# Kernel tuning notes

Measured on AMD Instinct MI355X. Metric: run time of the kernel, lower is better.

## Reference

```python
import jax, jax.numpy as jnp
import numpy as np

B, T, I, H, N, M, O = 256, 128, 512, 512, 1024, 512, 512
EPS = 1e-8


def setup_inputs() -> dict:
    key = jax.random.key(0)
    ks = jax.random.split(key, 10)
    rn = lambda k, shape, s: jax.random.normal(k, shape, jnp.float32) * s
    s_h, s_i, s_m = 1.0 / np.sqrt(H), 1.0 / np.sqrt(I), 1.0 / np.sqrt(M)
    return {
        "x": jax.random.normal(ks[0], (B, T, 1, I), jnp.float32),
        "mem0": jnp.full((N, M), 1e-6, jnp.float32),          # memory init fill_(1e-6)
        "wr0": jnp.eye(B, N, dtype=jnp.float32),               # torch.eye(batch, N)
        "ww0": jnp.eye(B, N, dtype=jnp.float32),
        "h0": rn(ks[1], (B, H), 1.0 / H),                      # normal_(0, 1/num_hidden)
        "Wx": rn(ks[2], (I, H), s_i),
        "Wr": rn(ks[3], (M, H), s_m),
        "bh": jnp.zeros((H,), jnp.float32),
        "Whr": rn(ks[4], (H, M + 6), s_h),                      # read head: k,beta,g,s(3),gamma
        "bhr": jnp.zeros((M + 6,), jnp.float32),
        "Whw": rn(ks[5], (H, M + 6), s_h),                      # write head addressing
        "bhw": jnp.zeros((M + 6,), jnp.float32),
        "Wea": rn(ks[6], (H, 2 * M), s_h),                      # write head erase/add
        "bea": jnp.zeros((2 * M,), jnp.float32),
        "Wo": rn(ks[7], (H, O), s_h),
        "bo": jnp.zeros((O,), jnp.float32),
    }


def _address(h, w_prev, mem, Wh, bh_):
    # Standard NTM addressing: content -> interpolate -> shift -> sharpen.
    p = h @ Wh + bh_                                   # (B, M+6)
    k = jnp.tanh(p[:, :M])                             # key (B, M)
    beta = jax.nn.softplus(p[:, M:M + 1])              # strength >= 0
    g = jax.nn.sigmoid(p[:, M + 1:M + 2])              # gate in (0,1)
    s = jax.nn.softmax(p[:, M + 2:M + 5], axis=-1)     # shift over {-1,0,+1}
    gamma = 1.0 + jax.nn.softplus(p[:, M + 5:M + 6])   # sharpen >= 1
    kn = k / (jnp.linalg.norm(k, axis=-1, keepdims=True) + EPS)
    mn = mem / (jnp.linalg.norm(mem, axis=-1, keepdims=True) + EPS)
    wc = jax.nn.softmax(beta * (kn @ mn.T), axis=-1)   # content weights (B, N)
    wg = g * wc + (1.0 - g) * w_prev                   # interpolation (strictly > 0)
    wt = (s[:, 0:1] * jnp.roll(wg, -1, axis=1)
          + s[:, 1:2] * wg
          + s[:, 2:3] * jnp.roll(wg, 1, axis=1))       # circular shift conv
    wp = wt ** gamma
    return wp / (jnp.sum(wp, axis=-1, keepdims=True) + EPS)


def reference(x, mem0, wr0, ww0, h0, Wx, Wr, bh, Whr, bhr, Whw, bhw, Wea, bea, Wo, bo):
    xs = jnp.transpose(x[:, :, 0, :], (1, 0, 2))       # (T, B, I): x.permute(1,0,2,3)

    def step(carry, x_t):
        mem, wr, ww, h = carry
        # write head (get_weights=False): erase/add into memory with prev ww
        ea = h @ Wea + bea
        e = jax.nn.sigmoid(ea[:, :M])                  # (B, M)
        a = jnp.tanh(ea[:, M:])                        # (B, M)
        mem = (mem * (1.0 - jnp.einsum('bn,bm->nm', ww, e) / B)
               + jnp.einsum('bn,bm->nm', ww, a) / B)   # batch-averaged, mem shared (N, M)
        # read head (get_weights=False): r = wr @ M
        r = wr @ mem                                   # (B, M)
        # controller.step(x_t, r)
        h = jnp.tanh(x_t @ Wx + r @ Wr + bh)           # (B, H)
        # new addressing weights from updated hidden + updated memory
        ww = _address(h, ww, mem, Whw, bhw)
        wr = _address(h, wr, mem, Whr, bhr)
        out = jax.nn.sigmoid(h @ Wo + bo)              # (B, O)
        return (mem, wr, ww, h), out

    _, outs = jax.lax.scan(step, (mem0, wr0, ww0, h0), xs)  # outs (T, B, O)
    return jnp.transpose(outs, (1, 0, 2))              # (B, T, O)
```

## Files before the change

kernel.cpp:

```cpp
#include <hip/hip_runtime.h>
#include <math.h>

#define B_ 256
#define T_ 128
#define I_ 512
#define H_ 512
#define N_ 1024
#define M_ 512
#define O_ 512
#define EPS_ 1e-8f

typedef unsigned short u16;
typedef __attribute__((ext_vector_type(8))) short v8s;
typedef __attribute__((ext_vector_type(4))) float v4f;

#define MFMA(a, b, c) __builtin_amdgcn_mfma_f32_16x16x32_bf16(a, b, c, 0, 0, 0)

#define PL_BIG 1310720
#define PL_WXT 262144
#define PL_WRT 262144
#define PL_MEM 524288
#define PL_W   262144
#define PL_H   131072
#define PL_KH  262144

__device__ __forceinline__ float sigm_(float x) { return 1.f / (1.f + expf(-x)); }
__device__ __forceinline__ float softplus_(float x) { return x > 20.f ? x : log1pf(expf(x)); }
__device__ __forceinline__ u16 f2bf(float f) {
    unsigned u = __float_as_uint(f);
    u += 0x7fffu + ((u >> 16) & 1u);
    return (u16)(u >> 16);
}
__device__ __forceinline__ float bf2f(u16 h) { return __uint_as_float((unsigned)h << 16); }
__device__ __forceinline__ void split2(float f, u16& h, u16& m) {
    h = f2bf(f);
    m = f2bf(f - bf2f(h));
}

__device__ __forceinline__ float wave_sum_(float v) {
#pragma unroll
    for (int o = 32; o > 0; o >>= 1) v += __shfl_down(v, o);
    return v;
}
__device__ __forceinline__ float wave_max_(float v) {
#pragma unroll
    for (int o = 32; o > 0; o >>= 1) v = fmaxf(v, __shfl_down(v, o));
    return v;
}
__device__ float block_sum_(float v, float* s) {
    int lane = threadIdx.x & 63, wid = threadIdx.x >> 6, nw = blockDim.x >> 6;
    v = wave_sum_(v);
    if (lane == 0) s[wid] = v;
    __syncthreads();
    float r = (threadIdx.x < nw) ? s[threadIdx.x] : 0.f;
    if (wid == 0) { r = wave_sum_(r); if (lane == 0) s[0] = r; }
    __syncthreads();
    float out = s[0];
    __syncthreads();
    return out;
}
__device__ float block_max_(float v, float* s) {
    int lane = threadIdx.x & 63, wid = threadIdx.x >> 6, nw = blockDim.x >> 6;
    v = wave_max_(v);
    if (lane == 0) s[wid] = v;
    __syncthreads();
    float r = (threadIdx.x < nw) ? s[threadIdx.x] : -3.4e38f;
    if (wid == 0) { r = wave_max_(r); if (lane == 0) s[0] = r; }
    __syncthreads();
    float out = s[0];
    __syncthreads();
    return out;
}

struct EpiEA0 {
    const float* bea; u16* eT; u16* aT;
    __device__ void operator()(int r0, int c, v4f v) const {
#pragma unroll
        for (int r = 0; r < 4; r++) {
            float val = v[r] + bea[c];
            u16* dst;
            int b = r0 + r;
            if (c < M_) { val = sigm_(val); dst = eT + (size_t)c * B_ + b; }
            else        { val = tanhf(val); dst = aT + (size_t)(c - M_) * B_ + b; }
            u16 h, m; split2(val, h, m);
            dst[0] = h; dst[PL_H] = m;
        }
    }
};
struct EpiR {
    u16* rp;
    __device__ void operator()(int r0, int c, v4f v) const {
#pragma unroll
        for (int r = 0; r < 4; r++) {
            u16 h, m; split2(v[r], h, m);
            size_t idx = (size_t)(r0 + r) * M_ + c;
            rp[idx] = h; rp[PL_H + idx] = m;
        }
    }
};
struct EpiH {
    const float* xwxt; const float* bh; float* hf; u16* hp;
    __device__ void operator()(int r0, int c, v4f v) const {
#pragma unroll
        for (int r = 0; r < 4; r++) {
            int b = r0 + r;
            float val = tanhf(v[r] + xwxt[(size_t)b * (T_ * O_) + c] + bh[c]);
            size_t idx = (size_t)b * H_ + c;
            hf[idx] = val;
            u16 h, m; split2(val, h, m);
            hp[idx] = h; hp[PL_H + idx] = m;
        }
    }
};
struct EpiFused {
    const float* bhw; const float* bhr; const float* bo; const float* bea;
    u16* khp; float* outt; u16* eT; u16* aT;
    __device__ void operator()(int r0, int c, v4f v) const {
        if (c < 1024) {
            int head = c >> 9, key = c & 511;
            const float* bb = head ? bhr : bhw;
#pragma unroll
            for (int r = 0; r < 4; r++) {
                float val = tanhf(v[r] + bb[key]);
                size_t idx = (size_t)(head * 256 + r0 + r) * M_ + key;
                u16 h, m; split2(val, h, m);
                khp[idx] = h; khp[PL_KH + idx] = m;
            }
        } else if (c < 1536) {
            int o = c - 1024;
#pragma unroll
            for (int r = 0; r < 4; r++)
                outt[(size_t)(r0 + r) * (T_ * O_) + o] = sigm_(v[r] + bo[o]);
        } else {
            int m = c - 1536;
#pragma unroll
            for (int r = 0; r < 4; r++) {
                float val = v[r] + bea[m];
                u16* dst;
                int b = r0 + r;
                if (m < M_) { val = sigm_(val); dst = eT + (size_t)m * B_ + b; }
                else        { val = tanhf(val); dst = aT + (size_t)(m - M_) * B_ + b; }
                u16 h, mm; split2(val, h, mm);
                dst[0] = h; dst[PL_H] = mm;
            }
        }
    }
};

template <int TM, class Epi>
__global__ __launch_bounds__(256) void gemm2(const u16* __restrict__ Ap, int lda, int apl,
                                             const u16* __restrict__ Bp, int ldb, int bpl,
                                             int K, Epi epi) {
    constexpr int AL = (TM * 32 * 2) / (256 * 8);
    constexpr int MT = TM / 32;
    __shared__ u16 As[2][TM][40];
    __shared__ u16 Bs[2][64][40];
    const int tid = threadIdx.x, lane = tid & 63, w = tid >> 6;
    const int wy = w >> 1, wx = w & 1, q = lane >> 4, l15 = lane & 15;
    const int row0 = blockIdx.y * TM, col0 = blockIdx.x * 64;
    uint4 ra[AL], rb[2];
    auto loadA = [&](int k0) {
#pragma unroll
        for (int j = 0; j < AL; j++) {
            int s = j * 256 + tid, p = s / (TM * 4), rr = (s >> 2) % TM, kg = s & 3;
            ra[j] = *(const uint4*)(Ap + (size_t)p * apl + (size_t)(row0 + rr) * lda + k0 + kg * 8);
        }
    };
    auto loadB = [&](int k0) {
#pragma unroll
        for (int j = 0; j < 2; j++) {
            int s = j * 256 + tid, p = s >> 8, rr = (s >> 2) & 63, kg = s & 3;
            rb[j] = *(const uint4*)(Bp + (size_t)p * bpl + (size_t)(col0 + rr) * ldb + k0 + kg * 8);
        }
    };
    v4f acc[MT][2] = {};
    loadA(0); loadB(0);
    for (int k0 = 0; k0 < K; k0 += 32) {
#pragma unroll
        for (int j = 0; j < AL; j++) {
            int s = j * 256 + tid, p = s / (TM * 4), rr = (s >> 2) % TM, kg = s & 3;
            *(uint4*)&As[p][rr][kg * 8] = ra[j];
        }
#pragma unroll
        for (int j = 0; j < 2; j++) {
            int s = j * 256 + tid, p = s >> 8, rr = (s >> 2) & 63, kg = s & 3;
            *(uint4*)&Bs[p][rr][kg * 8] = rb[j];
        }
        __syncthreads();
        if (k0 + 32 < K) { loadA(k0 + 32); loadB(k0 + 32); }
        v8s af[MT][2], bf[2][2];
#pragma unroll
        for (int mt = 0; mt < MT; mt++) {
            af[mt][0] = *(const v8s*)&As[0][wy * (TM / 2) + mt * 16 + l15][q * 8];
            af[mt][1] = *(const v8s*)&As[1][wy * (TM / 2) + mt * 16 + l15][q * 8];
        }
#pragma unroll
        for (int nt = 0; nt < 2; nt++) {
            bf[nt][0] = *(const v8s*)&Bs[0][wx * 32 + nt * 16 + l15][q * 8];
            bf[nt][1] = *(const v8s*)&Bs[1][wx * 32 + nt * 16 + l15][q * 8];
        }
#pragma unroll
        for (int mt = 0; mt < MT; mt++)
#pragma unroll
            for (int nt = 0; nt < 2; nt++) {
                v4f c = acc[mt][nt];
                c = MFMA(af[mt][0], bf[nt][0], c);
                c = MFMA(af[mt][0], bf[nt][1], c);
                c = MFMA(af[mt][1], bf[nt][0], c);
                acc[mt][nt] = c;
            }
        __syncthreads();
    }
#pragma unroll
    for (int mt = 0; mt < MT; mt++)
#pragma unroll
        for (int nt = 0; nt < 2; nt++)
            epi(row0 + wy * (TM / 2) + mt * 16 + q * 4, col0 + wx * 32 + nt * 16 + l15, acc[mt][nt]);
}

__global__ __launch_bounds__(256) void memupd2(const u16* __restrict__ wwT, const u16* __restrict__ eT,
                                               const u16* __restrict__ aT, float* __restrict__ memf,
                                               u16* __restrict__ mem_pl, u16* __restrict__ memT_pl,
                                               float* __restrict__ ssqp) {
    __shared__ u16 As[2][64][40], Be[2][64][40], Ba[2][64][40];
    __shared__ float ssqs[64];
    const int tid = threadIdx.x, lane = tid & 63, w = tid >> 6;
    const int wy = w >> 1, wx = w & 1, q = lane >> 4, l15 = lane & 15;
    const int row0 = blockIdx.y * 64, col0 = blockIdx.x * 64;
    if (tid < 64) ssqs[tid] = 0.f;
    uint4 rA[2], rE[2], rB[2];
    auto loadAll = [&](int k0) {
#pragma unroll
        for (int j = 0; j < 2; j++) {
            int s = j * 256 + tid, p = s >> 8, rr = (s >> 2) & 63, kg = s & 3;
            rA[j] = *(const uint4*)(wwT + (size_t)p * PL_W + (size_t)(row0 + rr) * B_ + k0 + kg * 8);
            rE[j] = *(const uint4*)(eT + (size_t)p * PL_H + (size_t)(col0 + rr) * B_ + k0 + kg * 8);
            rB[j] = *(const uint4*)(aT + (size_t)p * PL_H + (size_t)(col0 + rr) * B_ + k0 + kg * 8);
        }
    };
    v4f ae[2][2] = {}, aa[2][2] = {};
    loadAll(0);
    for (int k0 = 0; k0 < B_; k0 += 32) {
#pragma unroll
        for (int j = 0; j < 2; j++) {
            int s = j * 256 + tid, p = s >> 8, rr = (s >> 2) & 63, kg = s & 3;
            *(uint4*)&As[p][rr][kg * 8] = rA[j];
            *(uint4*)&Be[p][rr][kg * 8] = rE[j];
            *(uint4*)&Ba[p][rr][kg * 8] = rB[j];
        }
        __syncthreads();
        if (k0 + 32 < B_) loadAll(k0 + 32);
        v8s af[2][2], be[2][2], ba[2][2];
#pragma unroll
        for (int mt = 0; mt < 2; mt++) {
            af[mt][0] = *(const v8s*)&As[0][wy * 32 + mt * 16 + l15][q * 8];
            af[mt][1] = *(const v8s*)&As[1][wy * 32 + mt * 16 + l15][q * 8];
            be[mt][0] = *(const v8s*)&Be[0][wx * 32 + mt * 16 + l15][q * 8];
            be[mt][1] = *(const v8s*)&Be[1][wx * 32 + mt * 16 + l15][q * 8];
            ba[mt][0] = *(const v8s*)&Ba[0][wx * 32 + mt * 16 + l15][q * 8];
            ba[mt][1] = *(const v8s*)&Ba[1][wx * 32 + mt * 16 + l15][q * 8];
        }
#pragma unroll
        for (int mt = 0; mt < 2; mt++)
#pragma unroll
            for (int nt = 0; nt < 2; nt++) {
                v4f c = ae[mt][nt];
                c = MFMA(af[mt][0], be[nt][0], c);
                c = MFMA(af[mt][0], be[nt][1], c);
                c = MFMA(af[mt][1], be[nt][0], c);
                ae[mt][nt] = c;
                v4f d = aa[mt][nt];
                d = MFMA(af[mt][0], ba[nt][0], d);
                d = MFMA(af[mt][0], ba[nt][1], d);
                d = MFMA(af[mt][1], ba[nt][0], d);
                aa[mt][nt] = d;
            }
        __syncthreads();
    }
    const float invB = 1.f / (float)B_;
#pragma unroll
    for (int mt = 0; mt < 2; mt++)
#pragma unroll
        for (int nt = 0; nt < 2; nt++) {
            int r0 = row0 + wy * 32 + mt * 16 + q * 4;
            int c  = col0 + wx * 32 + nt * 16 + l15;
            u16 hv[4][2];
#pragma unroll
            for (int r = 0; r < 4; r++) {
                size_t idx = (size_t)(r0 + r) * M_ + c;
                float old = memf[idx];
                float nv = old * (1.f - ae[mt][nt][r] * invB) + aa[mt][nt][r] * invB;
                memf[idx] = nv;
                u16 h, m; split2(nv, h, m);
                mem_pl[idx] = h; mem_pl[PL_MEM + idx] = m;
                hv[r][0] = h; hv[r][1] = m;
                atomicAdd(&ssqs[r0 + r - row0], nv * nv);
            }
            size_t tb = (size_t)c * N_ + r0;
            *(ushort4*)&memT_pl[tb] = make_ushort4(hv[0][0], hv[1][0], hv[2][0], hv[3][0]);
            *(ushort4*)&memT_pl[PL_MEM + tb] = make_ushort4(hv[0][1], hv[1][1], hv[2][1], hv[3][1]);
        }
    __syncthreads();
    if (tid < 64) ssqp[(size_t)(row0 + tid) * 8 + blockIdx.x] = ssqs[tid];
}

__global__ __launch_bounds__(256) void logits2(const u16* __restrict__ khp, const u16* __restrict__ memp,
                                               const float* __restrict__ ssqp, float* __restrict__ logits) {
    __shared__ u16 As[2][64][40], Bs[2][64][40];
    __shared__ float invn_s[64];
    const int tid = threadIdx.x, lane = tid & 63, w = tid >> 6;
    const int wy = w >> 1, wx = w & 1, q = lane >> 4, l15 = lane & 15;
    const int row0 = blockIdx.y * 64, col0 = blockIdx.x * 64;
    if (tid < 64) {
        float s = 0.f;
#pragma unroll
        for (int j = 0; j < 8; j++) s += ssqp[(size_t)(col0 + tid) * 8 + j];
        invn_s[tid] = 1.f / (sqrtf(s) + EPS_);
    }
    uint4 ra[2], rb[2];
    auto loadAll = [&](int k0) {
#pragma unroll
        for (int j = 0; j < 2; j++) {
            int s = j * 256 + tid, p = s >> 8, rr = (s >> 2) & 63, kg = s & 3;
            ra[j] = *(const uint4*)(khp + (size_t)p * PL_KH + (size_t)(row0 + rr) * M_ + k0 + kg * 8);
            rb[j] = *(const uint4*)(memp + (size_t)p * PL_MEM + (size_t)(col0 + rr) * M_ + k0 + kg * 8);
        }
    };
    v4f acc[2][2] = {};
    loadAll(0);
    for (int k0 = 0; k0 < M_; k0 += 32) {
#pragma unroll
        for (int j = 0; j < 2; j++) {
            int s = j * 256 + tid, p = s >> 8, rr = (s >> 2) & 63, kg = s & 3;
            *(uint4*)&As[p][rr][kg * 8] = ra[j];
            *(uint4*)&Bs[p][rr][kg * 8] = rb[j];
        }
        __syncthreads();
        if (k0 + 32 < M_) loadAll(k0 + 32);
        v8s af[2][2], bf[2][2];
#pragma unroll
        for (int mt = 0; mt < 2; mt++) {
            af[mt][0] = *(const v8s*)&As[0][wy * 32 + mt * 16 + l15][q * 8];
            af[mt][1] = *(const v8s*)&As[1][wy * 32 + mt * 16 + l15][q * 8];
            bf[mt][0] = *(const v8s*)&Bs[0][wx * 32 + mt * 16 + l15][q * 8];
            bf[mt][1] = *(const v8s*)&Bs[1][wx * 32 + mt * 16 + l15][q * 8];
        }
#pragma unroll
        for (int mt = 0; mt < 2; mt++)
#pragma unroll
            for (int nt = 0; nt < 2; nt++) {
                v4f c = acc[mt][nt];
                c = MFMA(af[mt][0], bf[nt][0], c);
                c = MFMA(af[mt][0], bf[nt][1], c);
                c = MFMA(af[mt][1], bf[nt][0], c);
                acc[mt][nt] = c;
            }
        __syncthreads();
    }
#pragma unroll
    for (int mt = 0; mt < 2; mt++)
#pragma unroll
        for (int nt = 0; nt < 2; nt++) {
            int r0 = row0 + wy * 32 + mt * 16 + q * 4;
            int c  = col0 + wx * 32 + nt * 16 + l15;
            float in_ = invn_s[c - col0];
#pragma unroll
            for (int r = 0; r < 4; r++)
                logits[(size_t)(r0 + r) * N_ + c] = acc[mt][nt][r] * in_;
        }
}

__global__ __launch_bounds__(256) void gemm2_xwx(const float* __restrict__ x, const u16* __restrict__ WxT,
                                                 float* __restrict__ outbuf) {
    __shared__ u16 As[2][64][40];
    __shared__ u16 Bs[2][64][40];
    const int tid = threadIdx.x, lane = tid & 63, w = tid >> 6;
    const int wy = w >> 1, wx = w & 1, q = lane >> 4, l15 = lane & 15;
    const int row0 = blockIdx.y * 64, col0 = blockIdx.x * 64;
    const int sr = tid >> 2, ss = (tid & 3) * 8;
    const int arow = row0 + sr, ab = arow & 255, at = arow >> 8;
    const float* Asrc = x + ((size_t)ab * T_ + at) * I_ + ss;
    v4f acc[2][2] = {};
    for (int k0 = 0; k0 < I_; k0 += 32) {
        float4 f0 = *(const float4*)(Asrc + k0);
        float4 f1 = *(const float4*)(Asrc + k0 + 4);
        float av8[8] = {f0.x, f0.y, f0.z, f0.w, f1.x, f1.y, f1.z, f1.w};
#pragma unroll
        for (int j = 0; j < 8; j++) {
            u16 h, m; split2(av8[j], h, m);
            As[0][sr][ss + j] = h; As[1][sr][ss + j] = m;
        }
#pragma unroll
        for (int p = 0; p < 2; p++)
            *(uint4*)&Bs[p][sr][ss] = *(const uint4*)&WxT[(size_t)p * PL_WXT + (size_t)(col0 + sr) * I_ + k0 + ss];
        __syncthreads();
        v8s af[2][2], bf[2][2];
#pragma unroll
        for (int mt = 0; mt < 2; mt++) {
            af[mt][0] = *(const v8s*)&As[0][wy * 32 + mt * 16 + l15][q * 8];
            af[mt][1] = *(const v8s*)&As[1][wy * 32 + mt * 16 + l15][q * 8];
            bf[mt][0] = *(const v8s*)&Bs[0][wx * 32 + mt * 16 + l15][q * 8];
            bf[mt][1] = *(const v8s*)&Bs[1][wx * 32 + mt * 16 + l15][q * 8];
        }
#pragma unroll
        for (int mt = 0; mt < 2; mt++)
#pragma unroll
            for (int nt = 0; nt < 2; nt++) {
                v4f c = acc[mt][nt];
                c = MFMA(af[mt][0], bf[nt][0], c);
                c = MFMA(af[mt][0], bf[nt][1], c);
                c = MFMA(af[mt][1], bf[nt][0], c);
                acc[mt][nt] = c;
            }
        __syncthreads();
    }
#pragma unroll
    for (int mt = 0; mt < 2; mt++)
#pragma unroll
        for (int nt = 0; nt < 2; nt++) {
            int r0 = row0 + wy * 32 + mt * 16 + q * 4;
            int c  = col0 + wx * 32 + nt * 16 + l15;
#pragma unroll
            for (int r = 0; r < 4; r++) {
                int row = r0 + r, b = row & 255, t = row >> 8;
                outbuf[((size_t)b * T_ + t) * O_ + c] = acc[mt][nt][r];
            }
        }
}

__global__ __launch_bounds__(256) void decomp_t(const float* __restrict__ in, int ldin, int c0,
                                                int R, u16* __restrict__ outp, int opl) {
    __shared__ float Ls[32][33];
    const int r0 = blockIdx.x * 32, cB = blockIdx.y * 32;
    const int tid = threadIdx.x;
    int lr = tid >> 3, lc = (tid & 7) * 4;
#pragma unroll
    for (int j = 0; j < 4; j++)
        Ls[lr][lc + j] = in[(size_t)(r0 + lr) * ldin + c0 + cB + lc + j];
    __syncthreads();
    int lc2 = tid >> 3, lr2 = (tid & 7) * 4;
    u16 hv[4], mv[4];
#pragma unroll
    for (int j = 0; j < 4; j++) split2(Ls[lr2 + j][lc2], hv[j], mv[j]);
    size_t base = (size_t)(cB + lc2) * R + r0 + lr2;
    *(ushort4*)&outp[0 * (size_t)opl + base] = make_ushort4(hv[0], hv[1], hv[2], hv[3]);
    *(ushort4*)&outp[1 * (size_t)opl + base] = make_ushort4(mv[0], mv[1], mv[2], mv[3]);
}

__global__ __launch_bounds__(512) void wh6_kernel(const float* __restrict__ Whw, const float* __restrict__ Whr,
                                                  float* __restrict__ w6w, float* __restrict__ w6r) {
    int k = threadIdx.x;
    const float* src = blockIdx.x ? Whr : Whw;
    float* dst = blockIdx.x ? w6r : w6w;
#pragma unroll
    for (int j = 0; j < 6; j++) dst[k * 6 + j] = src[(size_t)k * (M_ + 6) + M_ + j];
}
__global__ __launch_bounds__(256) void init_mem(const float* __restrict__ mem0, float* __restrict__ memf,
                                                u16* __restrict__ mem_pl, u16* __restrict__ memT_pl) {
    int n = blockIdx.x;
    for (int c = threadIdx.x; c < M_; c += 256) {
        float v = mem0[(size_t)n * M_ + c];
        size_t idx = (size_t)n * M_ + c;
        memf[idx] = v;
        u16 h, m; split2(v, h, m);
        mem_pl[idx] = h; mem_pl[PL_MEM + idx] = m;
        size_t tb = (size_t)c * N_ + n;
        memT_pl[tb] = h; memT_pl[PL_MEM + tb] = m;
    }
}
__global__ __launch_bounds__(256) void init_w(const float* __restrict__ wr0, const float* __restrict__ ww0,
                                              float* __restrict__ wrf, float* __restrict__ wwf,
                                              u16* __restrict__ wr_pl, u16* __restrict__ wwT_pl) {
    int b = blockIdx.x;
    for (int n = threadIdx.x; n < N_; n += 256) {
        size_t idx = (size_t)b * N_ + n;
        float vw = ww0[idx]; wwf[idx] = vw;
        u16 h, m; split2(vw, h, m);
        size_t tb = (size_t)n * B_ + b;
        wwT_pl[tb] = h; wwT_pl[PL_W + tb] = m;
        float vr = wr0[idx]; wrf[idx] = vr;
        split2(vr, h, m);
        wr_pl[idx] = h; wr_pl[PL_W + idx] = m;
    }
}
__global__ __launch_bounds__(64) void init_h(const float* __restrict__ h0, float* __restrict__ hf,
                                             u16* __restrict__ hp) {
    int b = blockIdx.x;
    for (int c = threadIdx.x; c < H_; c += 64) {
        size_t idx = (size_t)b * H_ + c;
        float v = h0[idx];
        hf[idx] = v;
        u16 h, m; split2(v, h, m);
        hp[idx] = h; hp[PL_H + idx] = m;
    }
}

__global__ __launch_bounds__(256) void addr_k2(const float* __restrict__ logits, const float* __restrict__ hf,
                                               const float* __restrict__ w6w, const float* __restrict__ w6r,
                                               const float* __restrict__ bhw, const float* __restrict__ bhr,
                                               const u16* __restrict__ khp,
                                               float* __restrict__ wwf, float* __restrict__ wrf,
                                               u16* __restrict__ wwT_pl, u16* __restrict__ wr_pl) {
    __shared__ float wgs[N_];
    __shared__ float red[8];
    int row = blockIdx.x, head = row >> 8, b = row & 255;
    const float* w6 = head ? w6r : w6w;
    const float* bias = head ? bhr : bhw;
    float* wf = head ? wrf : wwf;
    int tid = threadIdx.x;
    float d0 = 0, d1 = 0, d2 = 0, d3 = 0, d4 = 0, d5 = 0, ssq = 0;
#pragma unroll
    for (int j = 0; j < 2; j++) {
        int k = tid + j * 256;
        float hv = hf[(size_t)b * H_ + k];
        const float* wk = w6 + k * 6;
        d0 += hv * wk[0]; d1 += hv * wk[1]; d2 += hv * wk[2];
        d3 += hv * wk[3]; d4 += hv * wk[4]; d5 += hv * wk[5];
        size_t ki = (size_t)row * M_ + k;
        float kv = bf2f(khp[ki]) + bf2f(khp[PL_KH + ki]);
        ssq += kv * kv;
    }
    d0 = block_sum_(d0, red); d1 = block_sum_(d1, red); d2 = block_sum_(d2, red);
    d3 = block_sum_(d3, red); d4 = block_sum_(d4, red); d5 = block_sum_(d5, red);
    ssq = block_sum_(ssq, red);
    float beta = softplus_(d0 + bias[M_]);
    float g = sigm_(d1 + bias[M_ + 1]);
    float a0 = d2 + bias[M_ + 2], a1 = d3 + bias[M_ + 3], a2 = d4 + bias[M_ + 4];
    float mx3 = fmaxf(a0, fmaxf(a1, a2));
    float e0 = expf(a0 - mx3), e1 = expf(a1 - mx3), e2 = expf(a2 - mx3);
    float es = e0 + e1 + e2;
    float s0 = e0 / es, s1 = e1 / es, s2 = e2 / es;
    float gamma = 1.f + softplus_(d5 + bias[M_ + 5]);
    float rowsc = beta / (sqrtf(ssq) + EPS_);
    float l[4];
#pragma unroll
    for (int j = 0; j < 4; j++) l[j] = logits[(size_t)row * N_ + tid * 4 + j] * rowsc;
    float mx = fmaxf(fmaxf(l[0], l[1]), fmaxf(l[2], l[3]));
    mx = block_max_(mx, red);
    float ex[4], sum = 0.f;
#pragma unroll
    for (int j = 0; j < 4; j++) { ex[j] = expf(l[j] - mx); sum += ex[j]; }
    sum = block_sum_(sum, red);
    float inv = 1.f / sum;
    float wprev[4];
#pragma unroll
    for (int j = 0; j < 4; j++) wprev[j] = wf[(size_t)b * N_ + tid * 4 + j];
#pragma unroll
    for (int j = 0; j < 4; j++) wgs[tid * 4 + j] = g * ex[j] * inv + (1.f - g) * wprev[j];
    __syncthreads();
    float wp[4], psum = 0.f;
#pragma unroll
    for (int j = 0; j < 4; j++) {
        int n = tid * 4 + j;
        float wt = s0 * wgs[(n + 1) & (N_ - 1)] + s1 * wgs[n] + s2 * wgs[(n - 1) & (N_ - 1)];
        float v = expf(gamma * logf(wt));
        wp[j] = v; psum += v;
    }
    psum = block_sum_(psum, red);
    float invp = 1.f / (psum + EPS_);
#pragma unroll
    for (int j = 0; j < 4; j++) {
        int n = tid * 4 + j;
        float val = wp[j] * invp;
        wf[(size_t)b * N_ + n] = val;
        u16 h, m; split2(val, h, m);
        if (head == 0) {
            size_t tb = (size_t)n * B_ + b;
            wwT_pl[tb] = h; wwT_pl[PL_W + tb] = m;
        } else {
            size_t idx = (size_t)b * N_ + n;
            wr_pl[idx] = h; wr_pl[PL_W + idx] = m;
        }
    }
}

extern "C" void kernel_launch(void* const* d_in, const int* in_sizes, int n_in,
                              void* d_out, int out_size, void* d_ws, size_t ws_size,
                              hipStream_t stream) {
    (void)in_sizes; (void)n_in; (void)out_size; (void)ws_size;
    const float* x    = (const float*)d_in[0];
    const float* mem0 = (const float*)d_in[1];
    const float* wr0  = (const float*)d_in[2];
    const float* ww0  = (const float*)d_in[3];
    const float* h0   = (const float*)d_in[4];
    const float* Wx   = (const float*)d_in[5];
    const float* Wr   = (const float*)d_in[6];
    const float* bh   = (const float*)d_in[7];
    const float* Whr  = (const float*)d_in[8];
    const float* bhr  = (const float*)d_in[9];
    const float* Whw  = (const float*)d_in[10];
    const float* bhw  = (const float*)d_in[11];
    const float* Wea  = (const float*)d_in[12];
    const float* bea  = (const float*)d_in[13];
    const float* Wo   = (const float*)d_in[14];
    const float* bo   = (const float*)d_in[15];
    float* out = (float*)d_out;

    char* wsb = (char*)d_ws;
    size_t off = 0;
    auto carveU = [&](size_t elems) { u16* p = (u16*)(wsb + off); off += elems * sizeof(u16); return p; };
    u16* BigT    = carveU(2 * (size_t)PL_BIG);
    u16* WxT     = carveU(2 * (size_t)PL_WXT);
    u16* WrT     = carveU(2 * (size_t)PL_WRT);
    u16* mem_pl  = carveU(2 * (size_t)PL_MEM);
    u16* memT_pl = carveU(2 * (size_t)PL_MEM);
    u16* wwT_pl  = carveU(2 * (size_t)PL_W);
    u16* wr_pl   = carveU(2 * (size_t)PL_W);
    u16* h_pl    = carveU(2 * (size_t)PL_H);
    u16* r_pl    = carveU(2 * (size_t)PL_H);
    u16* eT_pl   = carveU(2 * (size_t)PL_H);
    u16* aT_pl   = carveU(2 * (size_t)PL_H);
    u16* kh_pl   = carveU(2 * (size_t)PL_KH);
    auto carveF = [&](size_t elems) { float* p = (float*)(wsb + off); off += elems * sizeof(float); return p; };
    float* memf   = carveF((size_t)N_ * M_);
    float* wwf    = carveF((size_t)B_ * N_);
    float* wrf    = carveF((size_t)B_ * N_);
    float* hf     = carveF((size_t)B_ * H_);
    float* logits = carveF((size_t)2 * B_ * N_);
    float* ssqp   = carveF((size_t)N_ * 8);
    float* w6w    = carveF(H_ * 6);
    float* w6r    = carveF(H_ * 6);

    decomp_t<<<dim3(16, 16), 256, 0, stream>>>(Whw, M_ + 6, 0, 512, BigT, PL_BIG);
    decomp_t<<<dim3(16, 16), 256, 0, stream>>>(Whr, M_ + 6, 0, 512, BigT + (size_t)512 * 512, PL_BIG);
    decomp_t<<<dim3(16, 16), 256, 0, stream>>>(Wo, 512, 0, 512, BigT + (size_t)1024 * 512, PL_BIG);
    decomp_t<<<dim3(16, 32), 256, 0, stream>>>(Wea, 1024, 0, 512, BigT + (size_t)1536 * 512, PL_BIG);
    decomp_t<<<dim3(16, 16), 256, 0, stream>>>(Wx, 512, 0, 512, WxT, PL_WXT);
    decomp_t<<<dim3(16, 16), 256, 0, stream>>>(Wr, 512, 0, 512, WrT, PL_WRT);
    wh6_kernel<<<2, 512, 0, stream>>>(Whw, Whr, w6w, w6r);
    init_mem<<<N_, 256, 0, stream>>>(mem0, memf, mem_pl, memT_pl);
    init_w<<<B_, 256, 0, stream>>>(wr0, ww0, wrf, wwf, wr_pl, wwT_pl);
    init_h<<<B_, 64, 0, stream>>>(h0, hf, h_pl);
    gemm2_xwx<<<dim3(8, 512), 256, 0, stream>>>(x, WxT, out);
    gemm2<32, EpiEA0><<<dim3(16, 8), 256, 0, stream>>>(
        h_pl, 512, PL_H, BigT + (size_t)1536 * 512, 512, PL_BIG, 512, EpiEA0{bea, eT_pl, aT_pl});

    for (int t = 0; t < T_; t++) {
        memupd2<<<dim3(8, 16), 256, 0, stream>>>(wwT_pl, eT_pl, aT_pl, memf, mem_pl, memT_pl, ssqp);
        gemm2<32, EpiR><<<dim3(8, 8), 256, 0, stream>>>(
            wr_pl, 1024, PL_W, memT_pl, 1024, PL_MEM, 1024, EpiR{r_pl});
        gemm2<32, EpiH><<<dim3(8, 8), 256, 0, stream>>>(
            r_pl, 512, PL_H, WrT, 512, PL_WRT, 512, EpiH{out + (size_t)t * O_, bh, hf, h_pl});
        gemm2<32, EpiFused><<<dim3(40, 8), 256, 0, stream>>>(
            h_pl, 512, PL_H, BigT, 512, PL_BIG, 512,
            EpiFused{bhw, bhr, bo, bea, kh_pl, out + (size_t)t * O_, eT_pl, aT_pl});
        logits2<<<dim3(16, 8), 256, 0, stream>>>(kh_pl, mem_pl, ssqp, logits);
        addr_k2<<<2 * B_, 256, 0, stream>>>(logits, hf, w6w, w6r, bhw, bhr, kh_pl,
                                            wwf, wrf, wwT_pl, wr_pl);
    }
}
```

Baseline: 17.68 ms.

## Fuse per-step kernels into a cooperative persistent megakernel with grid syncs

Replaces the six kernel launches per timestep with one cooperative persistent kernel that runs six phases separated by grid-wide syncs, with a per-phase launch fallback. The r and h GEMMs become split-K tiles accumulated with atomics into fp32 buffers. The tanh for h is recomputed inside the consumer phases instead of being stored, and wr is split into bf16 planes on the fly. The aim is to remove launch overhead and raise parallelism for small per-step GEMMs. In exchange it adds grid-sync cost, atomic traffic, and occupancy limits from the combined shared-memory footprint.

```diff
diff --git a/kernel.cpp b/kernel.cpp
--- a/kernel.cpp
+++ b/kernel.cpp
@@ -1,5 +1,8 @@
 #include <hip/hip_runtime.h>
+#include <hip/hip_cooperative_groups.h>
 #include <math.h>
+
+namespace cg = cooperative_groups;
 
 #define B_ 256
 #define T_ 128
@@ -36,6 +39,11 @@
     h = f2bf(f);
     m = f2bf(f - bf2f(h));
 }
+__device__ __forceinline__ void mfma3(v4f& c, v8s a0, v8s a1, v8s b0, v8s b1) {
+    c = MFMA(a0, b0, c);
+    c = MFMA(a0, b1, c);
+    c = MFMA(a1, b0, c);
+}
 
 __device__ __forceinline__ float wave_sum_(float v) {
 #pragma unroll
@@ -70,6 +78,422 @@
     float out = s[0];
     __syncthreads();
     return out;
+}
+
+struct Sh {
+    u16 sA[2 * 32 * 40];
+    u16 sB[2 * 64 * 40];
+    u16 sB2[2 * 64 * 40];
+    float wgs[N_];
+    float red[8];
+    float ssq[32];
+};
+
+struct MArgs {
+    const float *bea, *bh, *bhw, *bhr, *bo, *w6w, *w6r;
+    const u16 *BigT, *WrT;
+    u16 *mem_pl, *memT_pl, *wwT_pl, *eT, *aT, *kh;
+    float *memf, *wwf, *wrf, *r_acc, *h_acc, *xwx_cur, *logits, *ssqp, *outbuf;
+};
+
+__device__ void phase1(const MArgs& A, Sh& sh, int u, int t) {
+    const int tid = threadIdx.x;
+    if (u >= 256) {
+        int j = u - 256;
+        if (tid < 128) {
+            float4 z = make_float4(0.f, 0.f, 0.f, 0.f);
+            *(float4*)&A.r_acc[(size_t)j * 512 + tid * 4] = z;
+            *(float4*)&A.h_acc[(size_t)j * 512 + tid * 4] = z;
+            *(float4*)&A.xwx_cur[(size_t)j * 512 + tid * 4] =
+                *(const float4*)&A.outbuf[((size_t)j * T_ + t) * O_ + tid * 4];
+        }
+        return;
+    }
+    const int lane = tid & 63, w = tid >> 6, wy = w >> 1, wx = w & 1, q = lane >> 4, l15 = lane & 15;
+    const int n0 = (u >> 3) * 32, m0c = (u & 7) * 64;
+    if (tid < 32) sh.ssq[tid] = 0.f;
+    const int ap = tid >> 7, ar = (tid >> 2) & 31, akg = tid & 3;
+    uint4 pa, pb[2], pc[2];
+    auto ld = [&](int k0) {
+        pa = *(const uint4*)(A.wwT_pl + (size_t)ap * PL_W + (size_t)(n0 + ar) * B_ + k0 + akg * 8);
+#pragma unroll
+        for (int j = 0; j < 2; j++) {
+            int s = j * 256 + tid, p = s >> 8, rr = (s >> 2) & 63, kg = s & 3;
+            pb[j] = *(const uint4*)(A.eT + (size_t)p * PL_H + (size_t)(m0c + rr) * B_ + k0 + kg * 8);
+            pc[j] = *(const uint4*)(A.aT + (size_t)p * PL_H + (size_t)(m0c + rr) * B_ + k0 + kg * 8);
+        }
+    };
+    v4f ae[2] = {}, aa[2] = {};
+    ld(0);
+    for (int k0 = 0; k0 < B_; k0 += 32) {
+        *(uint4*)&sh.sA[(ap * 32 + ar) * 40 + akg * 8] = pa;
+#pragma unroll
+        for (int j = 0; j < 2; j++) {
+            int s = j * 256 + tid, p = s >> 8, rr = (s >> 2) & 63, kg = s & 3;
+            *(uint4*)&sh.sB[(p * 64 + rr) * 40 + kg * 8] = pb[j];
+            *(uint4*)&sh.sB2[(p * 64 + rr) * 40 + kg * 8] = pc[j];
+        }
+        __syncthreads();
+        if (k0 + 32 < B_) ld(k0 + 32);
+        v8s a0 = *(const v8s*)&sh.sA[(0 * 32 + wy * 16 + l15) * 40 + q * 8];
+        v8s a1 = *(const v8s*)&sh.sA[(1 * 32 + wy * 16 + l15) * 40 + q * 8];
+#pragma unroll
+        for (int nt = 0; nt < 2; nt++) {
+            int rb = wx * 32 + nt * 16 + l15;
+            v8s e0 = *(const v8s*)&sh.sB[(0 * 64 + rb) * 40 + q * 8];
+            v8s e1 = *(const v8s*)&sh.sB[(1 * 64 + rb) * 40 + q * 8];
+            v8s c0 = *(const v8s*)&sh.sB2[(0 * 64 + rb) * 40 + q * 8];
+            v8s c1 = *(const v8s*)&sh.sB2[(1 * 64 + rb) * 40 + q * 8];
+            mfma3(ae[nt], a0, a1, e0, e1);
+            mfma3(aa[nt], a0, a1, c0, c1);
+        }
+        __syncthreads();
+    }
+    const float invB = 1.f / 256.f;
+#pragma unroll
+    for (int nt = 0; nt < 2; nt++) {
+        int n = n0 + wy * 16 + q * 4;
+        int m = m0c + wx * 32 + nt * 16 + l15;
+        u16 hv[4][2];
+#pragma unroll
+        for (int r = 0; r < 4; r++) {
+            size_t idx = (size_t)(n + r) * M_ + m;
+            float old = A.memf[idx];
+            float nv = old * (1.f - ae[nt][r] * invB) + aa[nt][r] * invB;
+            A.memf[idx] = nv;
+            u16 h, mm; split2(nv, h, mm);
+            A.mem_pl[idx] = h; A.mem_pl[PL_MEM + idx] = mm;
+            hv[r][0] = h; hv[r][1] = mm;
+            atomicAdd(&sh.ssq[n + r - n0], nv * nv);
+        }
+        size_t tb = (size_t)m * N_ + n;
+        *(ushort4*)&A.memT_pl[tb] = make_ushort4(hv[0][0], hv[1][0], hv[2][0], hv[3][0]);
+        *(ushort4*)&A.memT_pl[PL_MEM + tb] = make_ushort4(hv[0][1], hv[1][1], hv[2][1], hv[3][1]);
+    }
+    __syncthreads();
+    if (tid < 32) A.ssqp[(size_t)(n0 + tid) * 8 + (u & 7)] = sh.ssq[tid];
+}
+
+__device__ void phase2(const MArgs& A, Sh& sh, int u) {
+    const int tid = threadIdx.x;
+    const int lane = tid & 63, w = tid >> 6, wy = w >> 1, wx = w & 1, q = lane >> 4, l15 = lane & 15;
+    const int tile = u >> 2, kc = u & 3;
+    const int b0 = (tile >> 3) * 32, m0c = (tile & 7) * 64, kb = kc * 256;
+    const int ar = tid >> 3, akg = tid & 7;
+    float4 fa; uint4 pb[2];
+    auto ld = [&](int k0) {
+        fa = *(const float4*)(A.wrf + (size_t)(b0 + ar) * N_ + k0 + akg * 4);
+#pragma unroll
+        for (int j = 0; j < 2; j++) {
+            int s = j * 256 + tid, p = s >> 8, rr = (s >> 2) & 63, kg = s & 3;
+            pb[j] = *(const uint4*)(A.memT_pl + (size_t)p * PL_MEM + (size_t)(m0c + rr) * N_ + k0 + kg * 8);
+        }
+    };
+    v4f acc[2] = {};
+    ld(kb);
+    for (int k0 = kb; k0 < kb + 256; k0 += 32) {
+        u16 h0, l0, h1, l1, h2, l2, h3, l3;
+        split2(fa.x, h0, l0); split2(fa.y, h1, l1); split2(fa.z, h2, l2); split2(fa.w, h3, l3);
+        *(ushort4*)&sh.sA[(0 * 32 + ar) * 40 + akg * 4] = make_ushort4(h0, h1, h2, h3);
+        *(ushort4*)&sh.sA[(1 * 32 + ar) * 40 + akg * 4] = make_ushort4(l0, l1, l2, l3);
+#pragma unroll
+        for (int j = 0; j < 2; j++) {
+            int s = j * 256 + tid, p = s >> 8, rr = (s >> 2) & 63, kg = s & 3;
+            *(uint4*)&sh.sB[(p * 64 + rr) * 40 + kg * 8] = pb[j];
+        }
+        __syncthreads();
+        if (k0 + 32 < kb + 256) ld(k0 + 32);
+        v8s a0 = *(const v8s*)&sh.sA[(0 * 32 + wy * 16 + l15) * 40 + q * 8];
+        v8s a1 = *(const v8s*)&sh.sA[(1 * 32 + wy * 16 + l15) * 40 + q * 8];
+#pragma unroll
+        for (int nt = 0; nt < 2; nt++) {
+            int rb = wx * 32 + nt * 16 + l15;
+            v8s b0v = *(const v8s*)&sh.sB[(0 * 64 + rb) * 40 + q * 8];
+            v8s b1v = *(const v8s*)&sh.sB[(1 * 64 + rb) * 40 + q * 8];
+            mfma3(acc[nt], a0, a1, b0v, b1v);
+        }
+        __syncthreads();
+    }
+#pragma unroll
+    for (int nt = 0; nt < 2; nt++)
+#pragma unroll
+        for (int r = 0; r < 4; r++)
+            atomicAdd(&A.r_acc[(size_t)(b0 + wy * 16 + q * 4 + r) * M_ + m0c + wx * 32 + nt * 16 + l15],
+                      acc[nt][r]);
+}
+
+__device__ void phase3(const MArgs& A, Sh& sh, int u) {
+    const int tid = threadIdx.x;
+    const int lane = tid & 63, w = tid >> 6, wy = w >> 1, wx = w & 1, q = lane >> 4, l15 = lane & 15;
+    const int tile = u >> 2, kc = u & 3;
+    const int b0 = (tile >> 3) * 32, h0c = (tile & 7) * 64, kb = kc * 128;
+    const int ar = tid >> 3, akg = tid & 7;
+    float4 fa; uint4 pb[2];
+    auto ld = [&](int k0) {
+        fa = *(const float4*)(A.r_acc + (size_t)(b0 + ar) * M_ + k0 + akg * 4);
+#pragma unroll
+        for (int j = 0; j < 2; j++) {
+            int s = j * 256 + tid, p = s >> 8, rr = (s >> 2) & 63, kg = s & 3;
+            pb[j] = *(const uint4*)(A.WrT + (size_t)p * PL_WRT + (size_t)(h0c + rr) * M_ + k0 + kg * 8);
+        }
+    };
+    v4f acc[2] = {};
+    ld(kb);
+    for (int k0 = kb; k0 < kb + 128; k0 += 32) {
+        u16 h0, l0, h1, l1, h2, l2, h3, l3;
+        split2(fa.x, h0, l0); split2(fa.y, h1, l1); split2(fa.z, h2, l2); split2(fa.w, h3, l3);
+        *(ushort4*)&sh.sA[(0 * 32 + ar) * 40 + akg * 4] = make_ushort4(h0, h1, h2, h3);
+        *(ushort4*)&sh.sA[(1 * 32 + ar) * 40 + akg * 4] = make_ushort4(l0, l1, l2, l3);
+#pragma unroll
+        for (int j = 0; j < 2; j++) {
+            int s = j * 256 + tid, p = s >> 8, rr = (s >> 2) & 63, kg = s & 3;
+            *(uint4*)&sh.sB[(p * 64 + rr) * 40 + kg * 8] = pb[j];
+        }
+        __syncthreads();
+        if (k0 + 32 < kb + 128) ld(k0 + 32);
+        v8s a0 = *(const v8s*)&sh.sA[(0 * 32 + wy * 16 + l15) * 40 + q * 8];
+        v8s a1 = *(const v8s*)&sh.sA[(1 * 32 + wy * 16 + l15) * 40 + q * 8];
+#pragma unroll
+        for (int nt = 0; nt < 2; nt++) {
+            int rb = wx * 32 + nt * 16 + l15;
+            v8s b0v = *(const v8s*)&sh.sB[(0 * 64 + rb) * 40 + q * 8];
+            v8s b1v = *(const v8s*)&sh.sB[(1 * 64 + rb) * 40 + q * 8];
+            mfma3(acc[nt], a0, a1, b0v, b1v);
+        }
+        __syncthreads();
+    }
+#pragma unroll
+    for (int nt = 0; nt < 2; nt++)
+#pragma unroll
+        for (int r = 0; r < 4; r++)
+            atomicAdd(&A.h_acc[(size_t)(b0 + wy * 16 + q * 4 + r) * H_ + h0c + wx * 32 + nt * 16 + l15],
+                      acc[nt][r]);
+}
+
+__device__ void phase4(const MArgs& A, Sh& sh, int u, int t) {
+    const int tid = threadIdx.x;
+    const int lane = tid & 63, w = tid >> 6, wy = w >> 1, wx = w & 1, q = lane >> 4, l15 = lane & 15;
+    const int b0 = (u & 7) * 32, c0 = (u >> 3) * 64;
+    const int ar = tid >> 3, akg = tid & 7;
+    float4 fh, fx, fb; uint4 pb[2];
+    auto ld = [&](int k0) {
+        fh = *(const float4*)(A.h_acc + (size_t)(b0 + ar) * H_ + k0 + akg * 4);
+        fx = *(const float4*)(A.xwx_cur + (size_t)(b0 + ar) * H_ + k0 + akg * 4);
+        fb = *(const float4*)(A.bh + k0 + akg * 4);
+#pragma unroll
+        for (int j = 0; j < 2; j++) {
+            int s = j * 256 + tid, p = s >> 8, rr = (s >> 2) & 63, kg = s & 3;
+            pb[j] = *(const uint4*)(A.BigT + (size_t)p * PL_BIG + (size_t)(c0 + rr) * H_ + k0 + kg * 8);
+        }
+    };
+    v4f acc[2] = {};
+    ld(0);
+    for (int k0 = 0; k0 < H_; k0 += 32) {
+        float v0 = tanhf(fh.x + fx.x + fb.x), v1 = tanhf(fh.y + fx.y + fb.y);
+        float v2 = tanhf(fh.z + fx.z + fb.z), v3 = tanhf(fh.w + fx.w + fb.w);
+        u16 h0, l0, h1, l1, h2, l2, h3, l3;
+        split2(v0, h0, l0); split2(v1, h1, l1); split2(v2, h2, l2); split2(v3, h3, l3);
+        *(ushort4*)&sh.sA[(0 * 32 + ar) * 40 + akg * 4] = make_ushort4(h0, h1, h2, h3);
+        *(ushort4*)&sh.sA[(1 * 32 + ar) * 40 + akg * 4] = make_ushort4(l0, l1, l2, l3);
+#pragma unroll
+        for (int j = 0; j < 2; j++) {
+            int s = j * 256 + tid, p = s >> 8, rr = (s >> 2) & 63, kg = s & 3;
+            *(uint4*)&sh.sB[(p * 64 + rr) * 40 + kg * 8] = pb[j];
+        }
+        __syncthreads();
+        if (k0 + 32 < H_) ld(k0 + 32);
+        v8s a0 = *(const v8s*)&sh.sA[(0 * 32 + wy * 16 + l15) * 40 + q * 8];
+        v8s a1 = *(const v8s*)&sh.sA[(1 * 32 + wy * 16 + l15) * 40 + q * 8];
+#pragma unroll
+        for (int nt = 0; nt < 2; nt++) {
+            int rb = wx * 32 + nt * 16 + l15;
+            v8s b0v = *(const v8s*)&sh.sB[(0 * 64 + rb) * 40 + q * 8];
+            v8s b1v = *(const v8s*)&sh.sB[(1 * 64 + rb) * 40 + q * 8];
+            mfma3(acc[nt], a0, a1, b0v, b1v);
+        }
+        __syncthreads();
+    }
+#pragma unroll
+    for (int nt = 0; nt < 2; nt++) {
+        int c = c0 + wx * 32 + nt * 16 + l15;
+        int bb = b0 + wy * 16 + q * 4;
+        if (c < 1024) {
+            int head = c >> 9, key = c & 511;
+            const float* bias = head ? A.bhr : A.bhw;
+#pragma unroll
+            for (int r = 0; r < 4; r++) {
+                float val = tanhf(acc[nt][r] + bias[key]);
+                size_t idx = (size_t)(head * 256 + bb + r) * M_ + key;
+                u16 h, m; split2(val, h, m);
+                A.kh[idx] = h; A.kh[PL_KH + idx] = m;
+            }
+        } else if (c < 1536) {
+            int o = c - 1024;
+#pragma unroll
+            for (int r = 0; r < 4; r++)
+                A.outbuf[((size_t)(bb + r) * T_ + t) * O_ + o] = sigm_(acc[nt][r] + A.bo[o]);
+        } else {
+            int m = c - 1536;
+#pragma unroll
+            for (int r = 0; r < 4; r++) {
+                float val = acc[nt][r] + A.bea[m];
+                u16* dst;
+                if (m < M_) { val = sigm_(val); dst = A.eT + (size_t)m * B_ + bb + r; }
+                else        { val = tanhf(val); dst = A.aT + (size_t)(m - M_) * B_ + bb + r; }
+                u16 h, mm; split2(val, h, mm);
+                dst[0] = h; dst[PL_H] = mm;
+            }
+        }
+    }
+}
+
+__device__ void phase5(const MArgs& A, Sh& sh, int u) {
+    const int tid = threadIdx.x;
+    const int lane = tid & 63, w = tid >> 6, wy = w >> 1, wx = w & 1, q = lane >> 4, l15 = lane & 15;
+    const int r0 = (u >> 4) * 32, n0 = (u & 15) * 64;
+    const int ap = tid >> 7, ar = (tid >> 2) & 31, akg = tid & 3;
+    uint4 pa, pb[2];
+    auto ld = [&](int k0) {
+        pa = *(const uint4*)(A.kh + (size_t)ap * PL_KH + (size_t)(r0 + ar) * M_ + k0 + akg * 8);
+#pragma unroll
+        for (int j = 0; j < 2; j++) {
+            int s = j * 256 + tid, p = s >> 8, rr = (s >> 2) & 63, kg = s & 3;
+            pb[j] = *(const uint4*)(A.mem_pl + (size_t)p * PL_MEM + (size_t)(n0 + rr) * M_ + k0 + kg * 8);
+        }
+    };
+    v4f acc[2] = {};
+    ld(0);
+    for (int k0 = 0; k0 < M_; k0 += 32) {
+        *(uint4*)&sh.sA[(ap * 32 + ar) * 40 + akg * 8] = pa;
+#pragma unroll
+        for (int j = 0; j < 2; j++) {
+            int s = j * 256 + tid, p = s >> 8, rr = (s >> 2) & 63, kg = s & 3;
+            *(uint4*)&sh.sB[(p * 64 + rr) * 40 + kg * 8] = pb[j];
+        }
+        __syncthreads();
+        if (k0 + 32 < M_) ld(k0 + 32);
+        v8s a0 = *(const v8s*)&sh.sA[(0 * 32 + wy * 16 + l15) * 40 + q * 8];
+        v8s a1 = *(const v8s*)&sh.sA[(1 * 32 + wy * 16 + l15) * 40 + q * 8];
+#pragma unroll
+        for (int nt = 0; nt < 2; nt++) {
+            int rb = wx * 32 + nt * 16 + l15;
+            v8s b0v = *(const v8s*)&sh.sB[(0 * 64 + rb) * 40 + q * 8];
+            v8s b1v = *(const v8s*)&sh.sB[(1 * 64 + rb) * 40 + q * 8];
+            mfma3(acc[nt], a0, a1, b0v, b1v);
+        }
+        __syncthreads();
+    }
+#pragma unroll
+    for (int nt = 0; nt < 2; nt++) {
+        int c = n0 + wx * 32 + nt * 16 + l15;
+        float s = 0.f;
+#pragma unroll
+        for (int j2 = 0; j2 < 8; j2++) s += A.ssqp[(size_t)c * 8 + j2];
+        float invn = 1.f / (sqrtf(s) + EPS_);
+        int rr0 = r0 + wy * 16 + q * 4;
+#pragma unroll
+        for (int r = 0; r < 4; r++)
+            A.logits[(size_t)(rr0 + r) * N_ + c] = acc[nt][r] * invn;
+    }
+}
+
+__device__ void phase6(const MArgs& A, Sh& sh, int row) {
+    const int tid = threadIdx.x;
+    const int head = row >> 8, b = row & 255;
+    const float* w6 = head ? A.w6r : A.w6w;
+    const float* bias = head ? A.bhr : A.bhw;
+    float* wf = head ? A.wrf : A.wwf;
+    float d0 = 0, d1 = 0, d2 = 0, d3 = 0, d4 = 0, d5 = 0, ssq = 0;
+#pragma unroll
+    for (int j = 0; j < 2; j++) {
+        int k = tid + j * 256;
+        float hv = tanhf(A.h_acc[(size_t)b * H_ + k] + A.xwx_cur[(size_t)b * H_ + k] + A.bh[k]);
+        const float* wk = w6 + k * 6;
+        d0 += hv * wk[0]; d1 += hv * wk[1]; d2 += hv * wk[2];
+        d3 += hv * wk[3]; d4 += hv * wk[4]; d5 += hv * wk[5];
+        size_t ki = (size_t)row * M_ + k;
+        float kv = bf2f(A.kh[ki]) + bf2f(A.kh[PL_KH + ki]);
+        ssq += kv * kv;
+    }
+    d0 = block_sum_(d0, sh.red); d1 = block_sum_(d1, sh.red); d2 = block_sum_(d2, sh.red);
+    d3 = block_sum_(d3, sh.red); d4 = block_sum_(d4, sh.red); d5 = block_sum_(d5, sh.red);
+    ssq = block_sum_(ssq, sh.red);
+    float beta = softplus_(d0 + bias[M_]);
+    float g = sigm_(d1 + bias[M_ + 1]);
+    float a0s = d2 + bias[M_ + 2], a1s = d3 + bias[M_ + 3], a2s = d4 + bias[M_ + 4];
+    float mx3 = fmaxf(a0s, fmaxf(a1s, a2s));
+    float e0 = expf(a0s - mx3), e1 = expf(a1s - mx3), e2 = expf(a2s - mx3);
+    float es = e0 + e1 + e2;
+    float s0 = e0 / es, s1 = e1 / es, s2 = e2 / es;
+    float gamma = 1.f + softplus_(d5 + bias[M_ + 5]);
+    float rowsc = beta / (sqrtf(ssq) + EPS_);
+    float4 lv = *(const float4*)&A.logits[(size_t)row * N_ + tid * 4];
+    float l[4] = {lv.x * rowsc, lv.y * rowsc, lv.z * rowsc, lv.w * rowsc};
+    float mx = fmaxf(fmaxf(l[0], l[1]), fmaxf(l[2], l[3]));
+    mx = block_max_(mx, sh.red);
+    float ex[4], sum = 0.f;
+#pragma unroll
+    for (int j = 0; j < 4; j++) { ex[j] = expf(l[j] - mx); sum += ex[j]; }
+    sum = block_sum_(sum, sh.red);
+    float inv = 1.f / sum;
+    float4 wpv = *(const float4*)&wf[(size_t)b * N_ + tid * 4];
+    float wprev[4] = {wpv.x, wpv.y, wpv.z, wpv.w};
+#pragma unroll
+    for (int j = 0; j < 4; j++) sh.wgs[tid * 4 + j] = g * ex[j] * inv + (1.f - g) * wprev[j];
+    __syncthreads();
+    float wp[4], psum = 0.f;
+#pragma unroll
+    for (int j = 0; j < 4; j++) {
+        int n = tid * 4 + j;
+        float wt = s0 * sh.wgs[(n + 1) & (N_ - 1)] + s1 * sh.wgs[n] + s2 * sh.wgs[(n - 1) & (N_ - 1)];
+        float v = expf(gamma * logf(wt));
+        wp[j] = v; psum += v;
+    }
+    psum = block_sum_(psum, sh.red);
+    float invp = 1.f / (psum + EPS_);
+#pragma unroll
+    for (int j = 0; j < 4; j++) {
+        int n = tid * 4 + j;
+        float val = wp[j] * invp;
+        wf[(size_t)b * N_ + n] = val;
+        if (head == 0) {
+            u16 h, m; split2(val, h, m);
+            size_t tb = (size_t)n * B_ + b;
+            A.wwT_pl[tb] = h; A.wwT_pl[PL_W + tb] = m;
+        }
+    }
+}
+
+__global__ __launch_bounds__(256, 2) void ntm_mega(MArgs A) {
+    cg::grid_group grid = cg::this_grid();
+    __shared__ Sh sh;
+    const int NB = gridDim.x;
+    for (int t = 0; t < T_; t++) {
+        for (int u = blockIdx.x; u < 512; u += NB) phase1(A, sh, u, t);
+        grid.sync();
+        for (int u = blockIdx.x; u < 256; u += NB) phase2(A, sh, u);
+        grid.sync();
+        for (int u = blockIdx.x; u < 256; u += NB) phase3(A, sh, u);
+        grid.sync();
+        for (int u = blockIdx.x; u < 320; u += NB) phase4(A, sh, u, t);
+        grid.sync();
+        for (int u = blockIdx.x; u < 256; u += NB) phase5(A, sh, u);
+        grid.sync();
+        for (int u = blockIdx.x; u < 512; u += NB) phase6(A, sh, u);
+        grid.sync();
+    }
+}
+
+__global__ __launch_bounds__(256) void ntm_phase(MArgs A, int t, int ph) {
+    __shared__ Sh sh;
+    switch (ph) {
+    case 1: for (int u = blockIdx.x; u < 512; u += gridDim.x) phase1(A, sh, u, t); break;
+    case 2: for (int u = blockIdx.x; u < 256; u += gridDim.x) phase2(A, sh, u); break;
+    case 3: for (int u = blockIdx.x; u < 256; u += gridDim.x) phase3(A, sh, u); break;
+    case 4: for (int u = blockIdx.x; u < 320; u += gridDim.x) phase4(A, sh, u, t); break;
+    case 5: for (int u = blockIdx.x; u < 256; u += gridDim.x) phase5(A, sh, u); break;
+    case 6: for (int u = blockIdx.x; u < 512; u += gridDim.x) phase6(A, sh, u); break;
+    }
 }
 
 struct EpiEA0 {
@@ -84,65 +508,6 @@
             else        { val = tanhf(val); dst = aT + (size_t)(c - M_) * B_ + b; }
             u16 h, m; split2(val, h, m);
             dst[0] = h; dst[PL_H] = m;
-        }
-    }
-};
-struct EpiR {
-    u16* rp;
-    __device__ void operator()(int r0, int c, v4f v) const {
-#pragma unroll
-        for (int r = 0; r < 4; r++) {
-            u16 h, m; split2(v[r], h, m);
-            size_t idx = (size_t)(r0 + r) * M_ + c;
-            rp[idx] = h; rp[PL_H + idx] = m;
-        }
-    }
-};
-struct EpiH {
-    const float* xwxt; const float* bh; float* hf; u16* hp;
-    __device__ void operator()(int r0, int c, v4f v) const {
-#pragma unroll
-        for (int r = 0; r < 4; r++) {
-            int b = r0 + r;
-            float val = tanhf(v[r] + xwxt[(size_t)b * (T_ * O_) + c] + bh[c]);
-            size_t idx = (size_t)b * H_ + c;
-            hf[idx] = val;
-            u16 h, m; split2(val, h, m);
-            hp[idx] = h; hp[PL_H + idx] = m;
-        }
-    }
-};
-struct EpiFused {
-    const float* bhw; const float* bhr; const float* bo; const float* bea;
-    u16* khp; float* outt; u16* eT; u16* aT;
-    __device__ void operator()(int r0, int c, v4f v) const {
-        if (c < 1024) {
-            int head = c >> 9, key = c & 511;
-            const float* bb = head ? bhr : bhw;
-#pragma unroll
-            for (int r = 0; r < 4; r++) {
-                float val = tanhf(v[r] + bb[key]);
-                size_t idx = (size_t)(head * 256 + r0 + r) * M_ + key;
-                u16 h, m; split2(val, h, m);
-                khp[idx] = h; khp[PL_KH + idx] = m;
-            }
-        } else if (c < 1536) {
-            int o = c - 1024;
-#pragma unroll
-            for (int r = 0; r < 4; r++)
-                outt[(size_t)(r0 + r) * (T_ * O_) + o] = sigm_(v[r] + bo[o]);
-        } else {
-            int m = c - 1536;
-#pragma unroll
-            for (int r = 0; r < 4; r++) {
-                float val = v[r] + bea[m];
-                u16* dst;
-                int b = r0 + r;
-                if (m < M_) { val = sigm_(val); dst = eT + (size_t)m * B_ + b; }
-                else        { val = tanhf(val); dst = aT + (size_t)(m - M_) * B_ + b; }
-                u16 h, mm; split2(val, h, mm);
-                dst[0] = h; dst[PL_H] = mm;
-            }
         }
     }
 };
@@ -216,158 +581,6 @@
 #pragma unroll
         for (int nt = 0; nt < 2; nt++)
             epi(row0 + wy * (TM / 2) + mt * 16 + q * 4, col0 + wx * 32 + nt * 16 + l15, acc[mt][nt]);
-}
-
-__global__ __launch_bounds__(256) void memupd2(const u16* __restrict__ wwT, const u16* __restrict__ eT,
-                                               const u16* __restrict__ aT, float* __restrict__ memf,
-                                               u16* __restrict__ mem_pl, u16* __restrict__ memT_pl,
-                                               float* __restrict__ ssqp) {
-    __shared__ u16 As[2][64][40], Be[2][64][40], Ba[2][64][40];
-    __shared__ float ssqs[64];
-    const int tid = threadIdx.x, lane = tid & 63, w = tid >> 6;
-    const int wy = w >> 1, wx = w & 1, q = lane >> 4, l15 = lane & 15;
-    const int row0 = blockIdx.y * 64, col0 = blockIdx.x * 64;
-    if (tid < 64) ssqs[tid] = 0.f;
-    uint4 rA[2], rE[2], rB[2];
-    auto loadAll = [&](int k0) {
-#pragma unroll
-        for (int j = 0; j < 2; j++) {
-            int s = j * 256 + tid, p = s >> 8, rr = (s >> 2) & 63, kg = s & 3;
-            rA[j] = *(const uint4*)(wwT + (size_t)p * PL_W + (size_t)(row0 + rr) * B_ + k0 + kg * 8);
-            rE[j] = *(const uint4*)(eT + (size_t)p * PL_H + (size_t)(col0 + rr) * B_ + k0 + kg * 8);
-            rB[j] = *(const uint4*)(aT + (size_t)p * PL_H + (size_t)(col0 + rr) * B_ + k0 + kg * 8);
-        }
-    };
-    v4f ae[2][2] = {}, aa[2][2] = {};
-    loadAll(0);
-    for (int k0 = 0; k0 < B_; k0 += 32) {
-#pragma unroll
-        for (int j = 0; j < 2; j++) {
-            int s = j * 256 + tid, p = s >> 8, rr = (s >> 2) & 63, kg = s & 3;
-            *(uint4*)&As[p][rr][kg * 8] = rA[j];
-            *(uint4*)&Be[p][rr][kg * 8] = rE[j];
-            *(uint4*)&Ba[p][rr][kg * 8] = rB[j];
-        }
-        __syncthreads();
-        if (k0 + 32 < B_) loadAll(k0 + 32);
-        v8s af[2][2], be[2][2], ba[2][2];
-#pragma unroll
-        for (int mt = 0; mt < 2; mt++) {
-            af[mt][0] = *(const v8s*)&As[0][wy * 32 + mt * 16 + l15][q * 8];
-            af[mt][1] = *(const v8s*)&As[1][wy * 32 + mt * 16 + l15][q * 8];
-            be[mt][0] = *(const v8s*)&Be[0][wx * 32 + mt * 16 + l15][q * 8];
-            be[mt][1] = *(const v8s*)&Be[1][wx * 32 + mt * 16 + l15][q * 8];
-            ba[mt][0] = *(const v8s*)&Ba[0][wx * 32 + mt * 16 + l15][q * 8];
-            ba[mt][1] = *(const v8s*)&Ba[1][wx * 32 + mt * 16 + l15][q * 8];
-        }
-#pragma unroll
-        for (int mt = 0; mt < 2; mt++)
-#pragma unroll
-            for (int nt = 0; nt < 2; nt++) {
-                v4f c = ae[mt][nt];
-                c = MFMA(af[mt][0], be[nt][0], c);
-                c = MFMA(af[mt][0], be[nt][1], c);
-                c = MFMA(af[mt][1], be[nt][0], c);
-                ae[mt][nt] = c;
-                v4f d = aa[mt][nt];
-                d = MFMA(af[mt][0], ba[nt][0], d);
-                d = MFMA(af[mt][0], ba[nt][1], d);
-                d = MFMA(af[mt][1], ba[nt][0], d);
-                aa[mt][nt] = d;
-            }
-        __syncthreads();
-    }
-    const float invB = 1.f / (float)B_;
-#pragma unroll
-    for (int mt = 0; mt < 2; mt++)
-#pragma unroll
-        for (int nt = 0; nt < 2; nt++) {
-            int r0 = row0 + wy * 32 + mt * 16 + q * 4;
-            int c  = col0 + wx * 32 + nt * 16 + l15;
-            u16 hv[4][2];
-#pragma unroll
-            for (int r = 0; r < 4; r++) {
-                size_t idx = (size_t)(r0 + r) * M_ + c;
-                float old = memf[idx];
-                float nv = old * (1.f - ae[mt][nt][r] * invB) + aa[mt][nt][r] * invB;
-                memf[idx] = nv;
-                u16 h, m; split2(nv, h, m);
-                mem_pl[idx] = h; mem_pl[PL_MEM + idx] = m;
-                hv[r][0] = h; hv[r][1] = m;
-                atomicAdd(&ssqs[r0 + r - row0], nv * nv);
-            }
-            size_t tb = (size_t)c * N_ + r0;
-            *(ushort4*)&memT_pl[tb] = make_ushort4(hv[0][0], hv[1][0], hv[2][0], hv[3][0]);
-            *(ushort4*)&memT_pl[PL_MEM + tb] = make_ushort4(hv[0][1], hv[1][1], hv[2][1], hv[3][1]);
-        }
-    __syncthreads();
-    if (tid < 64) ssqp[(size_t)(row0 + tid) * 8 + blockIdx.x] = ssqs[tid];
-}
-
-__global__ __launch_bounds__(256) void logits2(const u16* __restrict__ khp, const u16* __restrict__ memp,
-                                               const float* __restrict__ ssqp, float* __restrict__ logits) {
-    __shared__ u16 As[2][64][40], Bs[2][64][40];
-    __shared__ float invn_s[64];
-    const int tid = threadIdx.x, lane = tid & 63, w = tid >> 6;
-    const int wy = w >> 1, wx = w & 1, q = lane >> 4, l15 = lane & 15;
-    const int row0 = blockIdx.y * 64, col0 = blockIdx.x * 64;
-    if (tid < 64) {
-        float s = 0.f;
-#pragma unroll
-        for (int j = 0; j < 8; j++) s += ssqp[(size_t)(col0 + tid) * 8 + j];
-        invn_s[tid] = 1.f / (sqrtf(s) + EPS_);
-    }
-    uint4 ra[2], rb[2];
-    auto loadAll = [&](int k0) {
-#pragma unroll
-        for (int j = 0; j < 2; j++) {
-            int s = j * 256 + tid, p = s >> 8, rr = (s >> 2) & 63, kg = s & 3;
-            ra[j] = *(const uint4*)(khp + (size_t)p * PL_KH + (size_t)(row0 + rr) * M_ + k0 + kg * 8);
-            rb[j] = *(const uint4*)(memp + (size_t)p * PL_MEM + (size_t)(col0 + rr) * M_ + k0 + kg * 8);
-        }
-    };
-    v4f acc[2][2] = {};
-    loadAll(0);
-    for (int k0 = 0; k0 < M_; k0 += 32) {
-#pragma unroll
-        for (int j = 0; j < 2; j++) {
-            int s = j * 256 + tid, p = s >> 8, rr = (s >> 2) & 63, kg = s & 3;
-            *(uint4*)&As[p][rr][kg * 8] = ra[j];
-            *(uint4*)&Bs[p][rr][kg * 8] = rb[j];
-        }
-        __syncthreads();
-        if (k0 + 32 < M_) loadAll(k0 + 32);
-        v8s af[2][2], bf[2][2];
-#pragma unroll
-        for (int mt = 0; mt < 2; mt++) {
-            af[mt][0] = *(const v8s*)&As[0][wy * 32 + mt * 16 + l15][q * 8];
-            af[mt][1] = *(const v8s*)&As[1][wy * 32 + mt * 16 + l15][q * 8];
-            bf[mt][0] = *(const v8s*)&Bs[0][wx * 32 + mt * 16 + l15][q * 8];
-            bf[mt][1] = *(const v8s*)&Bs[1][wx * 32 + mt * 16 + l15][q * 8];
-        }
-#pragma unroll
-        for (int mt = 0; mt < 2; mt++)
-#pragma unroll
-            for (int nt = 0; nt < 2; nt++) {
-                v4f c = acc[mt][nt];
-                c = MFMA(af[mt][0], bf[nt][0], c);
-                c = MFMA(af[mt][0], bf[nt][1], c);
-                c = MFMA(af[mt][1], bf[nt][0], c);
-                acc[mt][nt] = c;
-            }
-        __syncthreads();
-    }
-#pragma unroll
-    for (int mt = 0; mt < 2; mt++)
-#pragma unroll
-        for (int nt = 0; nt < 2; nt++) {
-            int r0 = row0 + wy * 32 + mt * 16 + q * 4;
-            int c  = col0 + wx * 32 + nt * 16 + l15;
-            float in_ = invn_s[c - col0];
-#pragma unroll
-            for (int r = 0; r < 4; r++)
-                logits[(size_t)(r0 + r) * N_ + c] = acc[mt][nt][r] * in_;
-        }
 }
 
 __global__ __launch_bounds__(256) void gemm2_xwx(const float* __restrict__ x, const u16* __restrict__ WxT,
@@ -470,7 +683,7 @@
 }
 __global__ __launch_bounds__(256) void init_w(const float* __restrict__ wr0, const float* __restrict__ ww0,
                                               float* __restrict__ wrf, float* __restrict__ wwf,
-                                              u16* __restrict__ wr_pl, u16* __restrict__ wwT_pl) {
+                                              u16* __restrict__ wwT_pl) {
     int b = blockIdx.x;
     for (int n = threadIdx.x; n < N_; n += 256) {
         size_t idx = (size_t)b * N_ + n;
@@ -478,99 +691,15 @@
         u16 h, m; split2(vw, h, m);
         size_t tb = (size_t)n * B_ + b;
         wwT_pl[tb] = h; wwT_pl[PL_W + tb] = m;
-        float vr = wr0[idx]; wrf[idx] = vr;
-        split2(vr, h, m);
-        wr_pl[idx] = h; wr_pl[PL_W + idx] = m;
-    }
-}
-__global__ __launch_bounds__(64) void init_h(const float* __restrict__ h0, float* __restrict__ hf,
-                                             u16* __restrict__ hp) {
+        wrf[idx] = wr0[idx];
+    }
+}
+__global__ __launch_bounds__(64) void init_h(const float* __restrict__ h0, u16* __restrict__ hp) {
     int b = blockIdx.x;
     for (int c = threadIdx.x; c < H_; c += 64) {
         size_t idx = (size_t)b * H_ + c;
-        float v = h0[idx];
-        hf[idx] = v;
-        u16 h, m; split2(v, h, m);
+        u16 h, m; split2(h0[idx], h, m);
         hp[idx] = h; hp[PL_H + idx] = m;
-    }
-}
-
-__global__ __launch_bounds__(256) void addr_k2(const float* __restrict__ logits, const float* __restrict__ hf,
-                                               const float* __restrict__ w6w, const float* __restrict__ w6r,
-                                               const float* __restrict__ bhw, const float* __restrict__ bhr,
-                                               const u16* __restrict__ khp,
-                                               float* __restrict__ wwf, float* __restrict__ wrf,
-                                               u16* __restrict__ wwT_pl, u16* __restrict__ wr_pl) {
-    __shared__ float wgs[N_];
-    __shared__ float red[8];
-    int row = blockIdx.x, head = row >> 8, b = row & 255;
-    const float* w6 = head ? w6r : w6w;
-    const float* bias = head ? bhr : bhw;
-    float* wf = head ? wrf : wwf;
-    int tid = threadIdx.x;
-    float d0 = 0, d1 = 0, d2 = 0, d3 = 0, d4 = 0, d5 = 0, ssq = 0;
-#pragma unroll
-    for (int j = 0; j < 2; j++) {
-        int k = tid + j * 256;
-        float hv = hf[(size_t)b * H_ + k];
-        const float* wk = w6 + k * 6;
-        d0 += hv * wk[0]; d1 += hv * wk[1]; d2 += hv * wk[2];
-        d3 += hv * wk[3]; d4 += hv * wk[4]; d5 += hv * wk[5];
-        size_t ki = (size_t)row * M_ + k;
-        float kv = bf2f(khp[ki]) + bf2f(khp[PL_KH + ki]);
-        ssq += kv * kv;
-    }
-    d0 = block_sum_(d0, red); d1 = block_sum_(d1, red); d2 = block_sum_(d2, red);
-    d3 = block_sum_(d3, red); d4 = block_sum_(d4, red); d5 = block_sum_(d5, red);
-    ssq = block_sum_(ssq, red);
-    float beta = softplus_(d0 + bias[M_]);
-    float g = sigm_(d1 + bias[M_ + 1]);
-    float a0 = d2 + bias[M_ + 2], a1 = d3 + bias[M_ + 3], a2 = d4 + bias[M_ + 4];
-    float mx3 = fmaxf(a0, fmaxf(a1, a2));
-    float e0 = expf(a0 - mx3), e1 = expf(a1 - mx3), e2 = expf(a2 - mx3);
-    float es = e0 + e1 + e2;
-    float s0 = e0 / es, s1 = e1 / es, s2 = e2 / es;
-    float gamma = 1.f + softplus_(d5 + bias[M_ + 5]);
-    float rowsc = beta / (sqrtf(ssq) + EPS_);
-    float l[4];
-#pragma unroll
-    for (int j = 0; j < 4; j++) l[j] = logits[(size_t)row * N_ + tid * 4 + j] * rowsc;
-    float mx = fmaxf(fmaxf(l[0], l[1]), fmaxf(l[2], l[3]));
-    mx = block_max_(mx, red);
-    float ex[4], sum = 0.f;
-#pragma unroll
-    for (int j = 0; j < 4; j++) { ex[j] = expf(l[j] - mx); sum += ex[j]; }
-    sum = block_sum_(sum, red);
-    float inv = 1.f / sum;
-    float wprev[4];
-#pragma unroll
-    for (int j = 0; j < 4; j++) wprev[j] = wf[(size_t)b * N_ + tid * 4 + j];
-#pragma unroll
-    for (int j = 0; j < 4; j++) wgs[tid * 4 + j] = g * ex[j] * inv + (1.f - g) * wprev[j];
-    __syncthreads();
-    float wp[4], psum = 0.f;
-#pragma unroll
-    for (int j = 0; j < 4; j++) {
-        int n = tid * 4 + j;
-        float wt = s0 * wgs[(n + 1) & (N_ - 1)] + s1 * wgs[n] + s2 * wgs[(n - 1) & (N_ - 1)];
-        float v = expf(gamma * logf(wt));
-        wp[j] = v; psum += v;
-    }
-    psum = block_sum_(psum, red);
-    float invp = 1.f / (psum + EPS_);
-#pragma unroll
-    for (int j = 0; j < 4; j++) {
-        int n = tid * 4 + j;
-        float val = wp[j] * invp;
-        wf[(size_t)b * N_ + n] = val;
-        u16 h, m; split2(val, h, m);
-        if (head == 0) {
-            size_t tb = (size_t)n * B_ + b;
-            wwT_pl[tb] = h; wwT_pl[PL_W + tb] = m;
-        } else {
-            size_t idx = (size_t)b * N_ + n;
-            wr_pl[idx] = h; wr_pl[PL_W + idx] = m;
-        }
     }
 }
 
@@ -605,21 +734,21 @@
     u16* mem_pl  = carveU(2 * (size_t)PL_MEM);
     u16* memT_pl = carveU(2 * (size_t)PL_MEM);
     u16* wwT_pl  = carveU(2 * (size_t)PL_W);
-    u16* wr_pl   = carveU(2 * (size_t)PL_W);
     u16* h_pl    = carveU(2 * (size_t)PL_H);
-    u16* r_pl    = carveU(2 * (size_t)PL_H);
     u16* eT_pl   = carveU(2 * (size_t)PL_H);
     u16* aT_pl   = carveU(2 * (size_t)PL_H);
     u16* kh_pl   = carveU(2 * (size_t)PL_KH);
     auto carveF = [&](size_t elems) { float* p = (float*)(wsb + off); off += elems * sizeof(float); return p; };
-    float* memf   = carveF((size_t)N_ * M_);
-    float* wwf    = carveF((size_t)B_ * N_);
-    float* wrf    = carveF((size_t)B_ * N_);
-    float* hf     = carveF((size_t)B_ * H_);
-    float* logits = carveF((size_t)2 * B_ * N_);
-    float* ssqp   = carveF((size_t)N_ * 8);
-    float* w6w    = carveF(H_ * 6);
-    float* w6r    = carveF(H_ * 6);
+    float* memf    = carveF((size_t)N_ * M_);
+    float* wwf     = carveF((size_t)B_ * N_);
+    float* wrf     = carveF((size_t)B_ * N_);
+    float* r_acc   = carveF((size_t)B_ * M_);
+    float* h_acc   = carveF((size_t)B_ * H_);
+    float* xwx_cur = carveF((size_t)B_ * H_);
+    float* logits  = carveF((size_t)2 * B_ * N_);
+    float* ssqp    = carveF((size_t)N_ * 8);
+    float* w6w     = carveF(H_ * 6);
+    float* w6r     = carveF(H_ * 6);
 
     decomp_t<<<dim3(16, 16), 256, 0, stream>>>(Whw, M_ + 6, 0, 512, BigT, PL_BIG);
     decomp_t<<<dim3(16, 16), 256, 0, stream>>>(Whr, M_ + 6, 0, 512, BigT + (size_t)512 * 512, PL_BIG);
@@ -629,23 +758,34 @@
     decomp_t<<<dim3(16, 16), 256, 0, stream>>>(Wr, 512, 0, 512, WrT, PL_WRT);
     wh6_kernel<<<2, 512, 0, stream>>>(Whw, Whr, w6w, w6r);
     init_mem<<<N_, 256, 0, stream>>>(mem0, memf, mem_pl, memT_pl);
-    init_w<<<B_, 256, 0, stream>>>(wr0, ww0, wrf, wwf, wr_pl, wwT_pl);
-    init_h<<<B_, 64, 0, stream>>>(h0, hf, h_pl);
+    init_w<<<B_, 256, 0, stream>>>(wr0, ww0, wrf, wwf, wwT_pl);
+    init_h<<<B_, 64, 0, stream>>>(h0, h_pl);
     gemm2_xwx<<<dim3(8, 512), 256, 0, stream>>>(x, WxT, out);
     gemm2<32, EpiEA0><<<dim3(16, 8), 256, 0, stream>>>(
         h_pl, 512, PL_H, BigT + (size_t)1536 * 512, 512, PL_BIG, 512, EpiEA0{bea, eT_pl, aT_pl});
 
-    for (int t = 0; t < T_; t++) {
-        memupd2<<<dim3(8, 16), 256, 0, stream>>>(wwT_pl, eT_pl, aT_pl, memf, mem_pl, memT_pl, ssqp);
-        gemm2<32, EpiR><<<dim3(8, 8), 256, 0, stream>>>(
-            wr_pl, 1024, PL_W, memT_pl, 1024, PL_MEM, 1024, EpiR{r_pl});
-        gemm2<32, EpiH><<<dim3(8, 8), 256, 0, stream>>>(
-            r_pl, 512, PL_H, WrT, 512, PL_WRT, 512, EpiH{out + (size_t)t * O_, bh, hf, h_pl});
-        gemm2<32, EpiFused><<<dim3(40, 8), 256, 0, stream>>>(
-            h_pl, 512, PL_H, BigT, 512, PL_BIG, 512,
-            EpiFused{bhw, bhr, bo, bea, kh_pl, out + (size_t)t * O_, eT_pl, aT_pl});
-        logits2<<<dim3(16, 8), 256, 0, stream>>>(kh_pl, mem_pl, ssqp, logits);
-        addr_k2<<<2 * B_, 256, 0, stream>>>(logits, hf, w6w, w6r, bhw, bhr, kh_pl,
-                                            wwf, wrf, wwT_pl, wr_pl);
-    }
-}
+    MArgs ma;
+    ma.bea = bea; ma.bh = bh; ma.bhw = bhw; ma.bhr = bhr; ma.bo = bo; ma.w6w = w6w; ma.w6r = w6r;
+    ma.BigT = BigT; ma.WrT = WrT;
+    ma.mem_pl = mem_pl; ma.memT_pl = memT_pl; ma.wwT_pl = wwT_pl; ma.eT = eT_pl; ma.aT = aT_pl; ma.kh = kh_pl;
+    ma.memf = memf; ma.wwf = wwf; ma.wrf = wrf; ma.r_acc = r_acc; ma.h_acc = h_acc;
+    ma.xwx_cur = xwx_cur; ma.logits = logits; ma.ssqp = ssqp; ma.outbuf = out;
+
+    int maxB = 0;
+    hipError_t qerr = hipOccupancyMaxActiveBlocksPerMultiprocessor(&maxB, ntm_mega, 256, 0);
+    bool coop = false;
+    if (qerr == hipSuccess && maxB >= 1) {
+        int nb = (maxB >= 2) ? 512 : 256;
+        void* kargs[1] = {&ma};
+        hipError_t lerr = hipLaunchCooperativeKernel(ntm_mega, dim3(nb), dim3(256), kargs, 0, stream);
+        if (lerr == hipSuccess) coop = true;
+        else (void)hipGetLastError();
+    } else {
+        (void)hipGetLastError();
+    }
+    if (!coop) {
+        for (int t = 0; t < T_; t++)
+            for (int ph = 1; ph <= 6; ph++)
+                ntm_phase<<<512, 256, 0, stream>>>(ma, t, ph);
+    }
+}
```

After: 39.69 ms. 125% more time.
